# Performance work log

Hardware: AMD Instinct MI355X
Metric: run time of the kernel (lower is better)

## Reference

```python
import jax, jax.numpy as jnp
import numpy as np

NEG_SLOPE = 0.2  # PyG GATConv default negative_slope


def _gcn(x, W, b, src, dst, N):
    # PyG GCNConv: lin -> gcn_norm with self loops -> scatter-add -> bias
    h = x @ W
    loop = jnp.arange(N)
    s = jnp.concatenate([src, loop])
    d = jnp.concatenate([dst, loop])
    deg = jax.ops.segment_sum(jnp.ones(s.shape[0], x.dtype), d, num_segments=N)
    dinv = jnp.where(deg > 0, jax.lax.rsqrt(jnp.maximum(deg, 1e-12)), 0.0)
    norm = dinv[s] * dinv[d]  # [E+N]
    return jax.ops.segment_sum(norm[:, None] * h[s], d, num_segments=N) + b


def _gat(x, Wl, a_src, a_dst, We, a_e, b, src, dst, edge_attr, N):
    # PyG GATConv, heads=1, add_self_loops=True, fill_value='mean' for edge_attr
    h = x @ Wl                      # [N, D]
    als = h @ a_src                 # [N]
    ald = h @ a_dst                 # [N]
    loop = jnp.arange(N)
    cnt = jax.ops.segment_sum(jnp.ones(dst.shape[0], x.dtype), dst, num_segments=N)
    loop_attr = jax.ops.segment_sum(edge_attr, dst, num_segments=N) / jnp.maximum(cnt, 1.0)[:, None]
    s = jnp.concatenate([src, loop])
    d = jnp.concatenate([dst, loop])
    ea = jnp.concatenate([edge_attr, loop_attr], axis=0)  # [E+N, 1]
    ae = (ea @ We) @ a_e            # edge-attr attention logit, [E+N]
    alpha = jax.nn.leaky_relu(als[s] + ald[d] + ae, NEG_SLOPE)
    m = jax.ops.segment_max(alpha, d, num_segments=N)
    e = jnp.exp(alpha - m[d])
    z = jax.ops.segment_sum(e, d, num_segments=N)
    w = e / (z[d] + 1e-16)          # PyG softmax eps
    return jax.ops.segment_sum(w[:, None] * h[s], d, num_segments=N) + b


def setup_inputs():
    key = jax.random.key(0)
    ks = jax.random.split(key, 32)
    NUM_ENT, T, D = 150000, 250000, 128
    NUM_ATT, NUM_VAL = 1000, 250000
    E1, E2 = 1000000, 500000
    N = NUM_ENT + T
    h = jax.random.randint(ks[0], (T,), 0, NUM_ENT)
    v = jax.random.randint(ks[1], (T,), 0, NUM_VAL)
    a = jax.random.randint(ks[2], (T,), 0, NUM_ATT)
    inp = {}
    inp['attribute_triples'] = jnp.stack([h, v, a], axis=1)
    inp['ent_edges'] = jax.random.randint(ks[3], (E1, 2), 0, NUM_ENT)
    inp['ent_edge_labels'] = jax.random.normal(ks[4], (E1, 1), jnp.float32)
    inp['val_edges'] = jax.random.randint(ks[5], (E2, 2), 0, N)
    inp['val_edge_labels'] = jax.random.randint(ks[6], (E2,), 0, NUM_ATT)
    inp['att_feats'] = jax.random.normal(ks[7], (NUM_ATT, D), jnp.float32) * 0.1
    inp['val_feats'] = jax.random.normal(ks[8], (NUM_VAL, D), jnp.float32) * 0.1
    inp['ent_feats'] = jax.random.normal(ks[9], (NUM_ENT, D), jnp.float32) * 0.1
    sW = (2.0 / (3 * D)) ** 0.5  # xavier-ish for [2D, D]
    sL = (1.0 / D) ** 0.5
    inp['W'] = jax.random.normal(ks[10], (2 * D, D), jnp.float32) * sW
    inp['gcn1_W'] = jax.random.normal(ks[11], (D, D), jnp.float32) * sL
    inp['gcn1_b'] = jnp.zeros((D,), jnp.float32)
    inp['gcn2_W'] = jax.random.normal(ks[12], (D, D), jnp.float32) * sL
    inp['gcn2_b'] = jnp.zeros((D,), jnp.float32)
    for i, pre in enumerate(['gat1', 'gat2']):
        kk = jax.random.split(ks[13 + i], 5)
        inp[pre + '_Wl'] = jax.random.normal(kk[0], (D, D), jnp.float32) * sL
        inp[pre + '_asrc'] = jax.random.normal(kk[1], (D,), jnp.float32) * sL
        inp[pre + '_adst'] = jax.random.normal(kk[2], (D,), jnp.float32) * sL
        inp[pre + '_We'] = jax.random.normal(kk[3], (1, D), jnp.float32) * sL
        inp[pre + '_ae'] = jax.random.normal(kk[4], (D,), jnp.float32) * sL
        inp[pre + '_b'] = jnp.zeros((D,), jnp.float32)
    return inp


def reference(attribute_triples, ent_edges, ent_edge_labels, val_edges, val_edge_labels,
              att_feats, val_feats, ent_feats, W,
              gcn1_W, gcn1_b, gcn2_W, gcn2_b,
              gat1_Wl, gat1_asrc, gat1_adst, gat1_We, gat1_ae, gat1_b,
              gat2_Wl, gat2_asrc, gat2_adst, gat2_We, gat2_ae, gat2_b):
    val_idx = attribute_triples[:, 1]
    att_idx = attribute_triples[:, 2]
    num_ent = ent_feats.shape[0]
    val_features = jnp.concatenate([att_feats[att_idx], val_feats[val_idx]], axis=1) @ W
    nodes = jnp.concatenate([ent_feats, val_features], axis=0)
    N = nodes.shape[0]
    vs, vd = val_edges[:, 0], val_edges[:, 1]
    nodes = _gcn(nodes, gcn1_W, gcn1_b, vs, vd, N)
    nodes = _gcn(nodes, gcn2_W, gcn2_b, vs, vd, N)
    es, ed = ent_edges[:, 0], ent_edges[:, 1]
    g1 = _gat(nodes, gat1_Wl, gat1_asrc, gat1_adst, gat1_We, gat1_ae, gat1_b, es, ed, ent_edge_labels, N)
    g2 = _gat(nodes, gat2_Wl, gat2_asrc, gat2_adst, gat2_We, gat2_ae, gat2_b, es, ed, ent_edge_labels, N)
    nodes = g1 + g2
    return nodes[:num_ent] + ent_feats
```

## Files before the change

kernel.cpp:

```cpp
#include <hip/hip_runtime.h>
#include <hip/hip_bf16.h>

typedef __attribute__((ext_vector_type(8))) short short8;
typedef __attribute__((ext_vector_type(4))) float f32x4;

__device__ __forceinline__ float b2f(ushort u){ unsigned v = ((unsigned)u)<<16; float f; __builtin_memcpy(&f,&v,4); return f; }
__device__ __forceinline__ ushort f2b(float x){ __hip_bfloat16 h = __float2bfloat16(x); ushort u; __builtin_memcpy(&u,&h,2); return u; }
__device__ __forceinline__ float lrelu(float x){ return x >= 0.f ? x : 0.2f*x; }


__global__ void k_zero(int* degi, long N, int* cntE, float* loopS, long NE){
  long i = (long)blockIdx.x*256 + threadIdx.x;
  if (i < N) degi[i] = 0;
  if (i < NE) { cntE[i] = 0; loopS[i] = 0.f; }
}

__global__ void k_deg_val(const int* __restrict__ ve, long E2, int* degi){
  long e = (long)blockIdx.x*256 + threadIdx.x;
  if (e < E2) atomicAdd(&degi[ve[2*e+1]], 1);
}

__global__ void k_deg_ent(const int* __restrict__ ee, const float* __restrict__ lab, long E1, int* cntE, float* loopS){
  long e = (long)blockIdx.x*256 + threadIdx.x;
  if (e < E1){ int d = ee[2*e+1]; atomicAdd(&cntE[d],1); atomicAdd(&loopS[d], lab[e]); }
}

__global__ void k_dinv(const int* degi, float* dinv, long N, const int* cntE, const float* loopS, float* loopA, long NE){
  long n = (long)blockIdx.x*256 + threadIdx.x;
  if (n < N) dinv[n] = rsqrtf((float)(degi[n]+1));
  if (n < NE) loopA[n] = loopS[n] / fmaxf((float)cntE[n], 1.f);
}

__global__ void k_scan1(const int* __restrict__ deg, long L, int* __restrict__ ps, int* __restrict__ bsum){
  __shared__ int s[256];
  long base = (long)blockIdx.x*1024;
  int t = threadIdx.x;
  int v[4]; int sum = 0;
#pragma unroll
  for (int i=0;i<4;++i){ long idx = base + t*4 + i; v[i] = (idx<L) ? deg[idx] : 0; sum += v[i]; }
  s[t] = sum; __syncthreads();
  for (int off=1; off<256; off<<=1){
    int x = 0;
    if (t>=off) x = s[t-off];
    __syncthreads();
    if (t>=off) s[t] += x;
    __syncthreads();
  }
  int run = s[t] - sum;
#pragma unroll
  for (int i=0;i<4;++i){ long idx = base + t*4 + i; if (idx<L) ps[idx] = run; run += v[i]; }
  if (t==255) bsum[blockIdx.x] = s[255];
}

__global__ void k_scan2(const int* __restrict__ bsum, int* __restrict__ boff, int nb){
  __shared__ int s[512];
  int t = threadIdx.x;
  int v = (t<nb) ? bsum[t] : 0;
  s[t] = v; __syncthreads();
  for (int off=1; off<512; off<<=1){
    int x = 0;
    if (t>=off) x = s[t-off];
    __syncthreads();
    if (t>=off) s[t] += x;
    __syncthreads();
  }
  if (t<nb) boff[t] = s[t] - v;
}

__global__ void k_scan3(int* __restrict__ ps, int* __restrict__ cur, const int* __restrict__ boff, long L, int E){
  long i = (long)blockIdx.x*256 + threadIdx.x;
  if (i < L){ int v = ps[i] + boff[i>>10]; ps[i] = v; cur[i] = v; }
  if (i == L) ps[L] = E;
}

__global__ void k_scatter_val(const int* __restrict__ ve, long E2, const float* __restrict__ dinv,
                              int* __restrict__ cur, int2* __restrict__ pk){
  long e = (long)blockIdx.x*256 + threadIdx.x;
  if (e >= E2) return;
  int s = ve[2*e], d = ve[2*e+1];
  int pos = atomicAdd(&cur[d], 1);
  int2 p; p.x = s; p.y = __float_as_int(dinv[s]);
  pk[pos] = p;
}

__global__ void k_scatter_ent(const int* __restrict__ ee, const float* __restrict__ lab, long E1,
                              int* __restrict__ cur, int2* __restrict__ pk){
  long e = (long)blockIdx.x*256 + threadIdx.x;
  if (e >= E1) return;
  int s = ee[2*e], d = ee[2*e+1];
  int pos = atomicAdd(&cur[d], 1);
  int2 p; p.x = s; p.y = __float_as_int(lab[e]);
  pk[pos] = p;
}


__global__ void k_wvt(const float* __restrict__ W, ushort* __restrict__ Wvt){
  int o = blockIdx.x*256 + threadIdx.x; int k = o>>7, n = o&127;
  Wvt[n*128+k] = f2b(W[(128+k)*128+n]);
}

__global__ void k_mm128(const float* __restrict__ A, const float* __restrict__ B, float* __restrict__ C){
  int o = blockIdx.x*256 + threadIdx.x; int k = o>>7, n = o&127;
  float s = 0.f;
  for (int j=0;j<128;++j) s += A[k*128+j]*B[j*128+n];
  C[o] = s;
}

__global__ void k_mmt(const float* __restrict__ P, const float* __restrict__ Wl, ushort* __restrict__ Mt){
  int o = blockIdx.x*256 + threadIdx.x; int k = o>>7, n = o&127;
  float s = 0.f;
  for (int j=0;j<128;++j) s += P[k*128+j]*Wl[j*128+n];
  Mt[n*128+k] = f2b(s);
}

__global__ void k_uv(const float* g1b, const float* g2b, const float* G2,
                     const float* Wl1, const float* Wl2,
                     float* u1, float* v1, float* u2, float* v2){
  __shared__ float t[128];
  int n = threadIdx.x;
  float s = 0.f;
  for (int k=0;k<128;++k) s += g1b[k]*G2[k*128+n];
  t[n] = s; __syncthreads();
  float a=0.f,b=0.f,c=0.f,dd=0.f;
  for (int j=0;j<128;++j){
    float w1 = Wl1[j*128+n], w2 = Wl2[j*128+n];
    a += t[j]*w1; c += t[j]*w2; b += g2b[j]*w1; dd += g2b[j]*w2;
  }
  u1[n]=a; v1[n]=b; u2[n]=c; v2[n]=dd;
}

__global__ void k_csc(const float* We1, const float* ae1, const float* We2, const float* ae2, float* csc){
  int t = threadIdx.x;
  __shared__ float s1[128], s2[128];
  s1[t] = We1[t]*ae1[t];
  s2[t] = We2[t]*ae2[t];
  __syncthreads();
  for (int off=64; off>0; off>>=1){ if (t<off){ s1[t]+=s1[t+off]; s2[t]+=s2[t+off]; } __syncthreads(); }
  if (t==0){ csc[0]=s1[0]; csc[1]=s2[0]; }
}

__global__ void k_attP(const float* __restrict__ att, const float* __restrict__ W, float* attP, long NA){
  long o = (long)blockIdx.x*256 + threadIdx.x;
  if (o >= NA*128) return;
  long a = o>>7; int n = o&127;
  float s = 0.f;
  for (int j=0;j<128;++j) s += att[a*128+j]*W[j*128+n];
  attP[o] = s;
}

__global__ void k_cast(const float* __restrict__ in, ushort* __restrict__ out, long n4){
  long i = (long)blockIdx.x*256 + threadIdx.x;
  if (i >= n4) return;
  float4 v = ((const float4*)in)[i];
  ushort4 o; o.x=f2b(v.x); o.y=f2b(v.y); o.z=f2b(v.z); o.w=f2b(v.w);
  ((ushort4*)out)[i] = o;
}

template<bool AF32>
__global__ __launch_bounds__(256) void k_gemm(const void* __restrict__ Ap, const ushort* __restrict__ Bt,
                                              ushort* __restrict__ C, long M, int ostride, int ooff,
                                              const float* __restrict__ u, const float* __restrict__ v,
                                              const float* __restrict__ rs){
  __shared__ ushort As[128*128];
  __shared__ ushort Bs[128*128];
  int tid = threadIdx.x;
  long m0 = (long)blockIdx.x * 128;
  {
    const int4* Bg = (const int4*)Bt;
#pragma unroll
    for (int it=0; it<8; ++it){
      int chunk = tid + it*256;
      int row = chunk >> 4, c = chunk & 15;
      int4 vv = Bg[chunk];
      *(int4*)&Bs[(row<<7) + (((c ^ row) & 15)<<3)] = vv;
    }
  }
  if (AF32){
    const float4* Ag = (const float4*)Ap;
#pragma unroll
    for (int it=0; it<16; ++it){
      int chunk = tid + it*256;
      int row = chunk >> 5, q = chunk & 31;
      long grow = m0 + row;
      float4 vv = make_float4(0.f,0.f,0.f,0.f);
      if (grow < M) vv = Ag[grow*32 + q];
      ushort4 h; h.x=f2b(vv.x); h.y=f2b(vv.y); h.z=f2b(vv.z); h.w=f2b(vv.w);
      int c16 = q >> 1, half = q & 1;
      *(ushort4*)&As[(row<<7) + (((c16 ^ row)&15)<<3) + (half<<2)] = h;
    }
  } else {
    const int4* Ag = (const int4*)Ap;
#pragma unroll
    for (int it=0; it<8; ++it){
      int chunk = tid + it*256;
      int row = chunk >> 4, c = chunk & 15;
      long grow = m0 + row;
      int4 vv = make_int4(0,0,0,0);
      if (grow < M) vv = Ag[grow*16 + c];
      *(int4*)&As[(row<<7) + (((c ^ row)&15)<<3)] = vv;
    }
  }
  __syncthreads();
  int wave = tid >> 6, lane = tid & 63;
  int wm = (wave & 1) << 6, wn = (wave >> 1) << 6;
  int l15 = lane & 15, quad = lane >> 4;
  f32x4 acc[4][4] = {};
#pragma unroll
  for (int kk=0; kk<4; ++kk){
    int ch = (kk<<2) + quad;
    short8 a[4], b[4];
#pragma unroll
    for (int i=0;i<4;++i){ int r = wm + (i<<4) + l15; a[i] = *(const short8*)&As[(r<<7) + (((ch ^ r)&15)<<3)]; }
#pragma unroll
    for (int j=0;j<4;++j){ int r = wn + (j<<4) + l15; b[j] = *(const short8*)&Bs[(r<<7) + (((ch ^ r)&15)<<3)]; }
#pragma unroll
    for (int i=0;i<4;++i)
#pragma unroll
      for (int j=0;j<4;++j)
        acc[i][j] = __builtin_amdgcn_mfma_f32_16x16x32_bf16(a[i], b[j], acc[i][j], 0,0,0);
  }
#pragma unroll
  for (int i=0;i<4;++i){
#pragma unroll
    for (int r=0;r<4;++r){
      long grow = m0 + wm + (i<<4) + (quad<<2) + r;
      if (grow < M){
        float rsv = rs ? rs[grow] : 0.f;
#pragma unroll
        for (int j=0;j<4;++j){
          int col = wn + (j<<4) + l15;
          float x = acc[i][j][r];
          if (u) x += rsv*u[col] + v[col];
          C[grow*(long)ostride + ooff + col] = f2b(x);
        }
      }
    }
  }
}


__global__ void k_gather(const int* __restrict__ trip, const float* __restrict__ attP,
                         const ushort* __restrict__ valP, ushort* __restrict__ h0, long T, long NEnt){
  int w = threadIdx.x >> 6, lane = threadIdx.x & 63;
  long t = (long)blockIdx.x*4 + w;
  if (t >= T) return;
  int a = trip[3*t+2], v = trip[3*t+1];
  float2 ap = ((const float2*)(attP + (long)a*128))[lane];
  unsigned vp = ((const unsigned*)(valP + (long)v*128))[lane];
  ushort2 o;
  o.x = f2b(ap.x + b2f((ushort)(vp & 0xffff)));
  o.y = f2b(ap.y + b2f((ushort)(vp >> 16)));
  ((ushort2*)(h0 + (NEnt + t)*128))[lane] = o;
}

__global__ void k_agg(const int* __restrict__ rp, const int2* __restrict__ pk,
                      const ushort* __restrict__ h, const float* __restrict__ dinv,
                      ushort* __restrict__ outH, float* __restrict__ rs, long R){
  int w = threadIdx.x>>6, lane = threadIdx.x&63;
  long d = (long)blockIdx.x*4 + w;
  if (d >= R) return;
  int r0 = rp[d], r1 = rp[d+1], ne = r1 - r0;
  float dv = dinv[d];
  unsigned hv = ((const unsigned*)(h + d*128))[lane];
  float wE = 0.f; int srcc = 0;
  if (lane < ne){ int2 p = pk[r0 + lane]; srcc = p.x; wE = dv * __int_as_float(p.y); }
  float wself = dv*dv;
  float ax = wself*b2f((ushort)(hv&0xffff));
  float ay = wself*b2f((ushort)(hv>>16));
  float wsum = wself;
  int lim = ne < 64 ? ne : 64;
  for (int j = 0; j < lim; j += 4){
    int i1 = (j+1<lim)? j+1 : lim-1;
    int i2 = (j+2<lim)? j+2 : lim-1;
    int i3 = (j+3<lim)? j+3 : lim-1;
    float w0=__shfl(wE,j),   w1=__shfl(wE,i1),   w2=__shfl(wE,i2),   w3=__shfl(wE,i3);
    int   s0=__shfl(srcc,j), s1=__shfl(srcc,i1), s2=__shfl(srcc,i2), s3=__shfl(srcc,i3);
    if (j+1>=lim) w1 = 0.f;
    if (j+2>=lim) w2 = 0.f;
    if (j+3>=lim) w3 = 0.f;
    unsigned v0 = ((const unsigned*)(h + (long)s0*128))[lane];
    unsigned v1 = ((const unsigned*)(h + (long)s1*128))[lane];
    unsigned v2 = ((const unsigned*)(h + (long)s2*128))[lane];
    unsigned v3 = ((const unsigned*)(h + (long)s3*128))[lane];
    wsum += w0+w1+w2+w3;
    ax += w0*b2f((ushort)(v0&0xffff)) + w1*b2f((ushort)(v1&0xffff))
        + w2*b2f((ushort)(v2&0xffff)) + w3*b2f((ushort)(v3&0xffff));
    ay += w0*b2f((ushort)(v0>>16)) + w1*b2f((ushort)(v1>>16))
        + w2*b2f((ushort)(v2>>16)) + w3*b2f((ushort)(v3>>16));
  }
  for (int e = r0+64; e < r1; ++e){
    int2 p = pk[e];
    float wgt = dv * __int_as_float(p.y);
    unsigned sv = ((const unsigned*)(h + (long)p.x*128))[lane];
    ax += wgt * b2f((ushort)(sv&0xffff));
    ay += wgt * b2f((ushort)(sv>>16));
    wsum += wgt;
  }
  ushort2 o; o.x = f2b(ax); o.y = f2b(ay);
  ((ushort2*)(outH + d*128))[lane] = o;
  if (rs && lane==0) rs[d] = wsum;
}

__global__ void k_dots(const uint2* __restrict__ hgI,
                       const float* vs1, const float* vd1, const float* vs2, const float* vd2,
                       float2* __restrict__ alsP, float2* __restrict__ aldP, long R){
  int w = threadIdx.x>>6, lane = threadIdx.x&63;
  long n = (long)blockIdx.x*4 + w;
  if (n >= R) return;
  bool lo = lane < 32; int l = lo ? lane : lane-32;
  uint2 hv = hgI[n*64 + lane];
  float4 us = lo ? ((const float4*)vs1)[l] : ((const float4*)vs2)[l];
  float4 ud = lo ? ((const float4*)vd1)[l] : ((const float4*)vd2)[l];
  float h0 = b2f((ushort)(hv.x&0xffff)), h1 = b2f((ushort)(hv.x>>16));
  float h2 = b2f((ushort)(hv.y&0xffff)), h3 = b2f((ushort)(hv.y>>16));
  float ps = h0*us.x + h1*us.y + h2*us.z + h3*us.w;
  float pd = h0*ud.x + h1*ud.y + h2*ud.z + h3*ud.w;
  for (int o=16;o>0;o>>=1){ ps += __shfl_down(ps,o); pd += __shfl_down(pd,o); }
  if (lane==0) { alsP[n].x = ps; aldP[n].x = pd; }
  if (lane==32){ alsP[n].y = ps; aldP[n].y = pd; }
}

__global__ void k_gat_csr(const int* __restrict__ rp, const int2* __restrict__ pk,
      const uint2* __restrict__ hgI,
      const float2* __restrict__ alsP, const float2* __restrict__ aldP,
      const float* __restrict__ loopA, const float* __restrict__ csc,
      const float* __restrict__ b1, const float* __restrict__ b2v,
      const float* __restrict__ entf, float* __restrict__ out, long R){
  int w = threadIdx.x>>6, lane = threadIdx.x&63;
  long d = (long)blockIdx.x*4 + w;
  if (d >= R) return;
  int r0 = rp[d], r1 = rp[d+1], ne = r1 - r0;
  float c1 = csc[0], c2 = csc[1];
  float2 aldd = aldP[d];
  float2 alsd = alsP[d];
  float la = loopA[d];
  float a1s = lrelu(alsd.x + aldd.x + c1*la);
  float a2s = lrelu(alsd.y + aldd.y + c2*la);
  float a1c = -1e30f, a2c = -1e30f; int srcc = 0;
  if (lane < ne){
    int2 p = pk[r0+lane];
    float lab = __int_as_float(p.y);
    float2 av = alsP[p.x];
    a1c = lrelu(av.x + aldd.x + c1*lab);
    a2c = lrelu(av.y + aldd.y + c2*lab);
    srcc = p.x;
  }
  float m1 = a1c, m2 = a2c;
  for (int o=32;o>0;o>>=1){ m1 = fmaxf(m1,__shfl_down(m1,o)); m2 = fmaxf(m2,__shfl_down(m2,o)); }
  m1 = fmaxf(__shfl(m1,0), a1s); m2 = fmaxf(__shfl(m2,0), a2s);
  for (int base=64; base<ne; base+=64){
    int i = base+lane; float x1=-1e30f, x2=-1e30f;
    if (i<ne){ int2 p = pk[r0+i]; float lab = __int_as_float(p.y); float2 av = alsP[p.x];
      x1 = lrelu(av.x + aldd.x + c1*lab); x2 = lrelu(av.y + aldd.y + c2*lab); }
    for (int o=32;o>0;o>>=1){ x1 = fmaxf(x1,__shfl_down(x1,o)); x2 = fmaxf(x2,__shfl_down(x2,o)); }
    m1 = fmaxf(m1, __shfl(x1,0)); m2 = fmaxf(m2, __shfl(x2,0));
  }
  float e1s = __expf(a1s-m1), e2s = __expf(a2s-m2);
  float z1 = e1s, z2 = e2s;
  bool lo = lane < 32;
  uint2 hv = hgI[d*64 + lane];
  float ws0 = lo ? e1s : e2s;
  float ac0 = ws0*b2f((ushort)(hv.x&0xffff));
  float ac1 = ws0*b2f((ushort)(hv.x>>16));
  float ac2 = ws0*b2f((ushort)(hv.y&0xffff));
  float ac3 = ws0*b2f((ushort)(hv.y>>16));
  {
    float e1 = (lane<ne) ? __expf(a1c-m1) : 0.f;
    float e2 = (lane<ne) ? __expf(a2c-m2) : 0.f;
    int lim = ne < 64 ? ne : 64;
    for (int j = 0; j < lim; j += 4){
      int i1 = (j+1<lim)? j+1 : lim-1;
      int i2 = (j+2<lim)? j+2 : lim-1;
      int i3 = (j+3<lim)? j+3 : lim-1;
      float f1a=__shfl(e1,j),   f1b=__shfl(e1,i1),  f1c=__shfl(e1,i2),  f1d=__shfl(e1,i3);
      float f2a=__shfl(e2,j),   f2bb=__shfl(e2,i1), f2c=__shfl(e2,i2),  f2d=__shfl(e2,i3);
      int   sa=__shfl(srcc,j),  sb=__shfl(srcc,i1), sc=__shfl(srcc,i2), sd=__shfl(srcc,i3);
      if (j+1>=lim){ f1b = 0.f; f2bb = 0.f; }
      if (j+2>=lim){ f1c = 0.f; f2c = 0.f; }
      if (j+3>=lim){ f1d = 0.f; f2d = 0.f; }
      uint2 va = hgI[(long)sa*64 + lane];
      uint2 vb = hgI[(long)sb*64 + lane];
      uint2 vc = hgI[(long)sc*64 + lane];
      uint2 vd = hgI[(long)sd*64 + lane];
      z1 += f1a+f1b+f1c+f1d; z2 += f2a+f2bb+f2c+f2d;
      float fa = lo ? f1a : f2a, fb = lo ? f1b : f2bb, fc = lo ? f1c : f2c, fd = lo ? f1d : f2d;
      ac0 += fa*b2f((ushort)(va.x&0xffff)) + fb*b2f((ushort)(vb.x&0xffff))
           + fc*b2f((ushort)(vc.x&0xffff)) + fd*b2f((ushort)(vd.x&0xffff));
      ac1 += fa*b2f((ushort)(va.x>>16)) + fb*b2f((ushort)(vb.x>>16))
           + fc*b2f((ushort)(vc.x>>16)) + fd*b2f((ushort)(vd.x>>16));
      ac2 += fa*b2f((ushort)(va.y&0xffff)) + fb*b2f((ushort)(vb.y&0xffff))
           + fc*b2f((ushort)(vc.y&0xffff)) + fd*b2f((ushort)(vd.y&0xffff));
      ac3 += fa*b2f((ushort)(va.y>>16)) + fb*b2f((ushort)(vb.y>>16))
           + fc*b2f((ushort)(vc.y>>16)) + fd*b2f((ushort)(vd.y>>16));
    }
  }
  for (int base=64; base<ne; base+=64){
    int i = base+lane; float e1=0.f, e2=0.f; int src = 0;
    if (i<ne){ int2 p = pk[r0+i]; float lab = __int_as_float(p.y); float2 av = alsP[p.x];
      e1 = __expf(lrelu(av.x + aldd.x + c1*lab)-m1);
      e2 = __expf(lrelu(av.y + aldd.y + c2*lab)-m2);
      src = p.x; }
    int lim2 = (ne-base < 64) ? (ne-base) : 64;
    for (int j2=0;j2<lim2;++j2){
      float f1 = __shfl(e1,j2), f2 = __shfl(e2,j2); int sj = __shfl(src,j2);
      z1 += f1; z2 += f2;
      uint2 vv = hgI[(long)sj*64 + lane];
      float f = lo ? f1 : f2;
      ac0 += f*b2f((ushort)(vv.x&0xffff));
      ac1 += f*b2f((ushort)(vv.x>>16));
      ac2 += f*b2f((ushort)(vv.y&0xffff));
      ac3 += f*b2f((ushort)(vv.y>>16));
    }
  }
  float iz = lo ? 1.f/(z1+1e-16f) : 1.f/(z2+1e-16f);
  ac0 *= iz; ac1 *= iz; ac2 *= iz; ac3 *= iz;
  int pl = lane ^ 32;
  float p0 = __shfl(ac0, pl), p1 = __shfl(ac1, pl), p2 = __shfl(ac2, pl), p3 = __shfl(ac3, pl);
  if (lo){
    float4 bb1 = ((const float4*)b1)[lane];
    float4 bb2 = ((const float4*)b2v)[lane];
    float4 ef  = ((const float4*)(entf + d*128))[lane];
    float4 o;
    o.x = ac0 + p0 + bb1.x + bb2.x + ef.x;
    o.y = ac1 + p1 + bb1.y + bb2.y + ef.y;
    o.z = ac2 + p2 + bb1.z + bb2.z + ef.z;
    o.w = ac3 + p3 + bb1.w + bb2.w + ef.w;
    ((float4*)(out + d*128))[lane] = o;
  }
}


extern "C" void kernel_launch(void* const* d_in, const int* in_sizes, int n_in,
                              void* d_out, int out_size, void* d_ws, size_t ws_size,
                              hipStream_t stream) {
  const int*   trip = (const int*)d_in[0];
  const int*   ee   = (const int*)d_in[1];
  const float* eel  = (const float*)d_in[2];
  const int*   ve   = (const int*)d_in[3];
  const float* att  = (const float*)d_in[5];
  const float* valf = (const float*)d_in[6];
  const float* entf = (const float*)d_in[7];
  const float* W    = (const float*)d_in[8];
  const float* G1   = (const float*)d_in[9];
  const float* g1b  = (const float*)d_in[10];
  const float* G2   = (const float*)d_in[11];
  const float* g2b  = (const float*)d_in[12];
  const float* Wl1  = (const float*)d_in[13];
  const float* as1v = (const float*)d_in[14];
  const float* ad1v = (const float*)d_in[15];
  const float* We1  = (const float*)d_in[16];
  const float* ae1  = (const float*)d_in[17];
  const float* b1   = (const float*)d_in[18];
  const float* Wl2  = (const float*)d_in[19];
  const float* as2v = (const float*)d_in[20];
  const float* ad2v = (const float*)d_in[21];
  const float* We2  = (const float*)d_in[22];
  const float* ae2  = (const float*)d_in[23];
  const float* b2   = (const float*)d_in[24];

  long T    = in_sizes[0]/3;
  long E1   = in_sizes[1]/2;
  long E2   = in_sizes[3]/2;
  long NA   = in_sizes[5]/128;
  long NV   = in_sizes[6]/128;
  long NEnt = in_sizes[7]/128;
  long N    = NEnt + T;

  size_t off = 0;
  auto alloc = [&](size_t bytes)->char*{
    char* p = (char*)d_ws + off; off = (off + bytes + 255) & ~(size_t)255; return p;
  };
  ushort* nodes0 = (ushort*)alloc((size_t)N*128*2);
  ushort* y1     = (ushort*)alloc((size_t)N*128*2);
  ushort* y2     = (ushort*)alloc((size_t)NEnt*128*2);
  float*  attP   = (float*)alloc((size_t)NA*128*4);
  int*    degi   = (int*)alloc(N*4);
  float*  dinv   = (float*)alloc(N*4);
  int*    cntE   = (int*)alloc(NEnt*4);
  float*  loopS  = (float*)alloc(NEnt*4);
  float*  loopA  = (float*)alloc(NEnt*4);
  float2* alsP   = (float2*)alloc(NEnt*8);
  float2* aldP   = (float2*)alloc(NEnt*8);
  float*  rs     = (float*)alloc(NEnt*4);
  int*    rpV    = (int*)alloc((N+1)*4);
  int*    curV   = (int*)alloc(N*4);
  int2*   pkV    = (int2*)alloc((size_t)E2*8);
  int*    rpE    = (int*)alloc((NEnt+1)*4);
  int*    curE   = (int*)alloc(NEnt*4);
  int2*   pkE    = (int2*)alloc((size_t)E1*8);
  int*    bsumV  = (int*)alloc(512*4);
  int*    boffV  = (int*)alloc(512*4);
  int*    bsumE  = (int*)alloc(512*4);
  int*    boffE  = (int*)alloc(512*4);
  ushort* Wvt    = (ushort*)alloc(16384*2);
  float*  P      = (float*)alloc(16384*4);
  ushort* M1t    = (ushort*)alloc(16384*2);
  ushort* M2t    = (ushort*)alloc(16384*2);
  float*  u1     = (float*)alloc(128*4);
  float*  v1     = (float*)alloc(128*4);
  float*  u2     = (float*)alloc(128*4);
  float*  v2     = (float*)alloc(128*4);
  float*  csc    = (float*)alloc(256);

  ushort* valP = y1;
  ushort* hgI  = nodes0;

  auto cdiv = [](long a, long b)->int{ return (int)((a + b - 1)/b); };
  int nbV = cdiv(N, 1024), nbE = cdiv(NEnt, 1024);

  k_zero<<<cdiv(N,256),256,0,stream>>>(degi, N, cntE, loopS, NEnt);
  k_deg_val<<<cdiv(E2,256),256,0,stream>>>(ve, E2, degi);
  k_deg_ent<<<cdiv(E1,256),256,0,stream>>>(ee, eel, E1, cntE, loopS);
  k_dinv<<<cdiv(N,256),256,0,stream>>>(degi, dinv, N, cntE, loopS, loopA, NEnt);

  k_scan1<<<nbV,256,0,stream>>>(degi, N, rpV, bsumV);
  k_scan2<<<1,512,0,stream>>>(bsumV, boffV, nbV);
  k_scan3<<<cdiv(N+1,256),256,0,stream>>>(rpV, curV, boffV, N, (int)E2);
  k_scan1<<<nbE,256,0,stream>>>(cntE, NEnt, rpE, bsumE);
  k_scan2<<<1,512,0,stream>>>(bsumE, boffE, nbE);
  k_scan3<<<cdiv(NEnt+1,256),256,0,stream>>>(rpE, curE, boffE, NEnt, (int)E1);
  k_scatter_val<<<cdiv(E2,256),256,0,stream>>>(ve, E2, dinv, curV, pkV);
  k_scatter_ent<<<cdiv(E1,256),256,0,stream>>>(ee, eel, E1, curE, pkE);

  k_wvt<<<64,256,0,stream>>>(W, Wvt);
  k_mm128<<<64,256,0,stream>>>(G1, G2, P);
  k_mmt<<<64,256,0,stream>>>(P, Wl1, M1t);
  k_mmt<<<64,256,0,stream>>>(P, Wl2, M2t);
  k_uv<<<1,128,0,stream>>>(g1b, g2b, G2, Wl1, Wl2, u1, v1, u2, v2);
  k_csc<<<1,128,0,stream>>>(We1, ae1, We2, ae2, csc);
  k_attP<<<cdiv(NA*128,256),256,0,stream>>>(att, W, attP, NA);

  k_gemm<true><<<cdiv(NV,128),256,0,stream>>>(valf, Wvt, valP, NV, 128, 0, nullptr, nullptr, nullptr);
  k_cast<<<cdiv(NEnt*32,256),256,0,stream>>>(entf, nodes0, NEnt*32);
  k_gather<<<cdiv(T,4),256,0,stream>>>(trip, attP, valP, nodes0, T, NEnt);

  k_agg<<<cdiv(N,4),256,0,stream>>>(rpV, pkV, nodes0, dinv, y1, nullptr, N);
  k_agg<<<cdiv(NEnt,4),256,0,stream>>>(rpV, pkV, y1, dinv, y2, rs, NEnt);

  k_gemm<false><<<cdiv(NEnt,128),256,0,stream>>>(y2, M1t, (ushort*)hgI, NEnt, 256, 0,   u1, v1, rs);
  k_gemm<false><<<cdiv(NEnt,128),256,0,stream>>>(y2, M2t, (ushort*)hgI, NEnt, 256, 128, u2, v2, rs);

  k_dots<<<cdiv(NEnt,4),256,0,stream>>>((const uint2*)hgI, as1v, ad1v, as2v, ad2v, alsP, aldP, NEnt);
  k_gat_csr<<<cdiv(NEnt,4),256,0,stream>>>(rpE, pkE, (const uint2*)hgI, alsP, aldP,
                                           loopA, csc, b1, b2, entf, (float*)d_out, NEnt);
}
```

Before: 1.028 ms.

## Fuse attention dot products into GEMM epilogue and use half-wave GCN aggregation

The separate k_dots kernel is removed. The GAT source and destination attention logits are now computed in the k_gemm epilogue through shared-memory atomic reductions, which saves a full re-read of the hgI features. Separately, k_agg now gives each destination node 32 lanes that load uint2 (four bf16 values) instead of a full wavefront loading two values each, so one block handles twice as many nodes. The trade-offs are LDS atomics and an extra barrier in the GEMM, plus a smaller per-node shuffle window (32 neighbours before the serial fallback loop).

New measurement: 1.080 ms. +5.0%, slower.

```diff
diff --git a/kernel.cpp b/kernel.cpp
--- a/kernel.cpp
+++ b/kernel.cpp
@@ -160,11 +160,15 @@
 __global__ __launch_bounds__(256) void k_gemm(const void* __restrict__ Ap, const ushort* __restrict__ Bt,
                                               ushort* __restrict__ C, long M, int ostride, int ooff,
                                               const float* __restrict__ u, const float* __restrict__ v,
-                                              const float* __restrict__ rs){
+                                              const float* __restrict__ rs,
+                                              const float* __restrict__ asv, const float* __restrict__ adv,
+                                              float2* __restrict__ alsO, float2* __restrict__ aldO, int layer){
   __shared__ ushort As[128*128];
   __shared__ ushort Bs[128*128];
+  __shared__ float sAls[128], sAld[128];
   int tid = threadIdx.x;
   long m0 = (long)blockIdx.x * 128;
+  if (asv && tid < 128){ sAls[tid] = 0.f; sAld[tid] = 0.f; }
   {
     const int4* Bg = (const int4*)Bt;
 #pragma unroll
@@ -223,16 +227,30 @@
   for (int i=0;i<4;++i){
 #pragma unroll
     for (int r=0;r<4;++r){
-      long grow = m0 + wm + (i<<4) + (quad<<2) + r;
+      int lrow = wm + (i<<4) + (quad<<2) + r;
+      long grow = m0 + lrow;
       if (grow < M){
         float rsv = rs ? rs[grow] : 0.f;
+        float pAls = 0.f, pAld = 0.f;
 #pragma unroll
         for (int j=0;j<4;++j){
           int col = wn + (j<<4) + l15;
           float x = acc[i][j][r];
           if (u) x += rsv*u[col] + v[col];
+          if (asv){ pAls += x*asv[col]; pAld += x*adv[col]; }
           C[grow*(long)ostride + ooff + col] = f2b(x);
         }
+        if (asv){ atomicAdd(&sAls[lrow], pAls); atomicAdd(&sAld[lrow], pAld); }
+      }
+    }
+  }
+  if (asv){
+    __syncthreads();
+    if (tid < 128){
+      long grow = m0 + tid;
+      if (grow < M){
+        if (layer == 0){ alsO[grow].x = sAls[tid]; aldO[grow].x = sAld[tid]; }
+        else           { alsO[grow].y = sAls[tid]; aldO[grow].y = sAld[tid]; }
       }
     }
   }
@@ -256,68 +274,58 @@
 __global__ void k_agg(const int* __restrict__ rp, const int2* __restrict__ pk,
                       const ushort* __restrict__ h, const float* __restrict__ dinv,
                       ushort* __restrict__ outH, float* __restrict__ rs, long R){
-  int w = threadIdx.x>>6, lane = threadIdx.x&63;
-  long d = (long)blockIdx.x*4 + w;
+  int g = threadIdx.x>>5, l = threadIdx.x&31;
+  long d = (long)blockIdx.x*8 + g;
   if (d >= R) return;
+  int base = (g&1)<<5;
   int r0 = rp[d], r1 = rp[d+1], ne = r1 - r0;
   float dv = dinv[d];
-  unsigned hv = ((const unsigned*)(h + d*128))[lane];
+  uint2 hv = ((const uint2*)(h + d*128))[l];
   float wE = 0.f; int srcc = 0;
-  if (lane < ne){ int2 p = pk[r0 + lane]; srcc = p.x; wE = dv * __int_as_float(p.y); }
+  if (l < ne){ int2 p = pk[r0 + l]; srcc = p.x; wE = dv * __int_as_float(p.y); }
   float wself = dv*dv;
-  float ax = wself*b2f((ushort)(hv&0xffff));
-  float ay = wself*b2f((ushort)(hv>>16));
+  float a0 = wself*b2f((ushort)(hv.x&0xffff));
+  float a1 = wself*b2f((ushort)(hv.x>>16));
+  float a2 = wself*b2f((ushort)(hv.y&0xffff));
+  float a3 = wself*b2f((ushort)(hv.y>>16));
   float wsum = wself;
-  int lim = ne < 64 ? ne : 64;
+  int lim = ne < 32 ? ne : 32;
   for (int j = 0; j < lim; j += 4){
     int i1 = (j+1<lim)? j+1 : lim-1;
     int i2 = (j+2<lim)? j+2 : lim-1;
     int i3 = (j+3<lim)? j+3 : lim-1;
-    float w0=__shfl(wE,j),   w1=__shfl(wE,i1),   w2=__shfl(wE,i2),   w3=__shfl(wE,i3);
-    int   s0=__shfl(srcc,j), s1=__shfl(srcc,i1), s2=__shfl(srcc,i2), s3=__shfl(srcc,i3);
+    float w0=__shfl(wE,base+j),   w1=__shfl(wE,base+i1),   w2=__shfl(wE,base+i2),   w3=__shfl(wE,base+i3);
+    int   s0=__shfl(srcc,base+j), s1=__shfl(srcc,base+i1), s2=__shfl(srcc,base+i2), s3=__shfl(srcc,base+i3);
     if (j+1>=lim) w1 = 0.f;
     if (j+2>=lim) w2 = 0.f;
     if (j+3>=lim) w3 = 0.f;
-    unsigned v0 = ((const unsigned*)(h + (long)s0*128))[lane];
-    unsigned v1 = ((const unsigned*)(h + (long)s1*128))[lane];
-    unsigned v2 = ((const unsigned*)(h + (long)s2*128))[lane];
-    unsigned v3 = ((const unsigned*)(h + (long)s3*128))[lane];
+    uint2 v0 = ((const uint2*)(h + (long)s0*128))[l];
+    uint2 v1 = ((const uint2*)(h + (long)s1*128))[l];
+    uint2 v2 = ((const uint2*)(h + (long)s2*128))[l];
+    uint2 v3 = ((const uint2*)(h + (long)s3*128))[l];
     wsum += w0+w1+w2+w3;
-    ax += w0*b2f((ushort)(v0&0xffff)) + w1*b2f((ushort)(v1&0xffff))
-        + w2*b2f((ushort)(v2&0xffff)) + w3*b2f((ushort)(v3&0xffff));
-    ay += w0*b2f((ushort)(v0>>16)) + w1*b2f((ushort)(v1>>16))
-        + w2*b2f((ushort)(v2>>16)) + w3*b2f((ushort)(v3>>16));
-  }
-  for (int e = r0+64; e < r1; ++e){
+    a0 += w0*b2f((ushort)(v0.x&0xffff)) + w1*b2f((ushort)(v1.x&0xffff))
+        + w2*b2f((ushort)(v2.x&0xffff)) + w3*b2f((ushort)(v3.x&0xffff));
+    a1 += w0*b2f((ushort)(v0.x>>16)) + w1*b2f((ushort)(v1.x>>16))
+        + w2*b2f((ushort)(v2.x>>16)) + w3*b2f((ushort)(v3.x>>16));
+    a2 += w0*b2f((ushort)(v0.y&0xffff)) + w1*b2f((ushort)(v1.y&0xffff))
+        + w2*b2f((ushort)(v2.y&0xffff)) + w3*b2f((ushort)(v3.y&0xffff));
+    a3 += w0*b2f((ushort)(v0.y>>16)) + w1*b2f((ushort)(v1.y>>16))
+        + w2*b2f((ushort)(v2.y>>16)) + w3*b2f((ushort)(v3.y>>16));
+  }
+  for (int e = r0+32; e < r1; ++e){
     int2 p = pk[e];
     float wgt = dv * __int_as_float(p.y);
-    unsigned sv = ((const unsigned*)(h + (long)p.x*128))[lane];
-    ax += wgt * b2f((ushort)(sv&0xffff));
-    ay += wgt * b2f((ushort)(sv>>16));
+    uint2 sv = ((const uint2*)(h + (long)p.x*128))[l];
+    a0 += wgt * b2f((ushort)(sv.x&0xffff));
+    a1 += wgt * b2f((ushort)(sv.x>>16));
+    a2 += wgt * b2f((ushort)(sv.y&0xffff));
+    a3 += wgt * b2f((ushort)(sv.y>>16));
     wsum += wgt;
   }
-  ushort2 o; o.x = f2b(ax); o.y = f2b(ay);
-  ((ushort2*)(outH + d*128))[lane] = o;
-  if (rs && lane==0) rs[d] = wsum;
-}
-
-__global__ void k_dots(const uint2* __restrict__ hgI,
-                       const float* vs1, const float* vd1, const float* vs2, const float* vd2,
-                       float2* __restrict__ alsP, float2* __restrict__ aldP, long R){
-  int w = threadIdx.x>>6, lane = threadIdx.x&63;
-  long n = (long)blockIdx.x*4 + w;
-  if (n >= R) return;
-  bool lo = lane < 32; int l = lo ? lane : lane-32;
-  uint2 hv = hgI[n*64 + lane];
-  float4 us = lo ? ((const float4*)vs1)[l] : ((const float4*)vs2)[l];
-  float4 ud = lo ? ((const float4*)vd1)[l] : ((const float4*)vd2)[l];
-  float h0 = b2f((ushort)(hv.x&0xffff)), h1 = b2f((ushort)(hv.x>>16));
-  float h2 = b2f((ushort)(hv.y&0xffff)), h3 = b2f((ushort)(hv.y>>16));
-  float ps = h0*us.x + h1*us.y + h2*us.z + h3*us.w;
-  float pd = h0*ud.x + h1*ud.y + h2*ud.z + h3*ud.w;
-  for (int o=16;o>0;o>>=1){ ps += __shfl_down(ps,o); pd += __shfl_down(pd,o); }
-  if (lane==0) { alsP[n].x = ps; aldP[n].x = pd; }
-  if (lane==32){ alsP[n].y = ps; aldP[n].y = pd; }
+  ushort4 o; o.x = f2b(a0); o.y = f2b(a1); o.z = f2b(a2); o.w = f2b(a3);
+  ((ushort4*)(outH + d*128))[l] = o;
+  if (rs && l==0) rs[d] = wsum;
 }
 
 __global__ void k_gat_csr(const int* __restrict__ rp, const int2* __restrict__ pk,
@@ -530,17 +538,19 @@
   k_csc<<<1,128,0,stream>>>(We1, ae1, We2, ae2, csc);
   k_attP<<<cdiv(NA*128,256),256,0,stream>>>(att, W, attP, NA);
 
-  k_gemm<true><<<cdiv(NV,128),256,0,stream>>>(valf, Wvt, valP, NV, 128, 0, nullptr, nullptr, nullptr);
+  k_gemm<true><<<cdiv(NV,128),256,0,stream>>>(valf, Wvt, valP, NV, 128, 0, nullptr, nullptr, nullptr,
+                                              nullptr, nullptr, nullptr, nullptr, 0);
   k_cast<<<cdiv(NEnt*32,256),256,0,stream>>>(entf, nodes0, NEnt*32);
   k_gather<<<cdiv(T,4),256,0,stream>>>(trip, attP, valP, nodes0, T, NEnt);
 
-  k_agg<<<cdiv(N,4),256,0,stream>>>(rpV, pkV, nodes0, dinv, y1, nullptr, N);
-  k_agg<<<cdiv(NEnt,4),256,0,stream>>>(rpV, pkV, y1, dinv, y2, rs, NEnt);
-
-  k_gemm<false><<<cdiv(NEnt,128),256,0,stream>>>(y2, M1t, (ushort*)hgI, NEnt, 256, 0,   u1, v1, rs);
-  k_gemm<false><<<cdiv(NEnt,128),256,0,stream>>>(y2, M2t, (ushort*)hgI, NEnt, 256, 128, u2, v2, rs);
-
-  k_dots<<<cdiv(NEnt,4),256,0,stream>>>((const uint2*)hgI, as1v, ad1v, as2v, ad2v, alsP, aldP, NEnt);
+  k_agg<<<cdiv(N,8),256,0,stream>>>(rpV, pkV, nodes0, dinv, y1, nullptr, N);
+  k_agg<<<cdiv(NEnt,8),256,0,stream>>>(rpV, pkV, y1, dinv, y2, rs, NEnt);
+
+  k_gemm<false><<<cdiv(NEnt,128),256,0,stream>>>(y2, M1t, (ushort*)hgI, NEnt, 256, 0,   u1, v1, rs,
+                                                 as1v, ad1v, alsP, aldP, 0);
+  k_gemm<false><<<cdiv(NEnt,128),256,0,stream>>>(y2, M2t, (ushort*)hgI, NEnt, 256, 128, u2, v2, rs,
+                                                 as2v, ad2v, alsP, aldP, 1);
+
   k_gat_csr<<<cdiv(NEnt,4),256,0,stream>>>(rpE, pkE, (const uint2*)hgI, alsP, aldP,
                                            loopA, csc, b1, b2, entf, (float*)d_out, NEnt);
 }
```
